# Optimization experiments

Measured on AMD Instinct MI355X. Metric: run time of the kernel, lower is better.

The kernel has to match this reference:

```python
import jax, jax.numpy as jnp
import numpy as np

N_NODES = 100000
N_EDGES = 625000
HIDDEN = 128
N_LAYERS = 4
NUM_GRAPHS = 512
INPUT_DIM = 28
EDGE_DIM = 4
OUT_DIM = 1


def setup_inputs() -> dict:
    key = jax.random.key(0)
    ks = jax.random.split(key, 16)
    x = jax.random.randint(ks[0], (N_NODES, 1), 0, INPUT_DIM)
    edge_index = jax.random.randint(ks[1], (2, N_EDGES), 0, N_NODES)
    edge_attr = jax.random.randint(ks[2], (N_EDGES,), 0, EDGE_DIM)
    batch = jnp.sort(jax.random.randint(ks[3], (N_NODES,), 0, NUM_GRAPHS))
    s = 1.0 / np.sqrt(HIDDEN)
    node_emb = jax.random.normal(ks[4], (INPUT_DIM, HIDDEN), jnp.float32)
    edge_emb = jax.random.normal(ks[5], (EDGE_DIM, HIDDEN), jnp.float32)
    conv_W1 = jax.random.normal(ks[6], (N_LAYERS, HIDDEN, HIDDEN), jnp.float32) * s
    conv_b1 = jnp.zeros((N_LAYERS, HIDDEN), jnp.float32)
    conv_W2 = jax.random.normal(ks[7], (N_LAYERS, HIDDEN, HIDDEN), jnp.float32) * s
    conv_b2 = jnp.zeros((N_LAYERS, HIDDEN), jnp.float32)
    mlp_W1 = jax.random.normal(ks[8], (HIDDEN, HIDDEN // 2), jnp.float32) * s
    mlp_b1 = jnp.zeros((HIDDEN // 2,), jnp.float32)
    mlp_W2 = jax.random.normal(ks[9], (HIDDEN // 2, HIDDEN // 4), jnp.float32) * (1.0 / np.sqrt(HIDDEN // 2))
    mlp_b2 = jnp.zeros((HIDDEN // 4,), jnp.float32)
    mlp_W3 = jax.random.normal(ks[10], (HIDDEN // 4, OUT_DIM), jnp.float32) * (1.0 / np.sqrt(HIDDEN // 4))
    mlp_b3 = jnp.zeros((OUT_DIM,), jnp.float32)
    return dict(x=x, edge_index=edge_index, edge_attr=edge_attr, batch=batch,
                node_emb=node_emb, edge_emb=edge_emb,
                conv_W1=conv_W1, conv_b1=conv_b1, conv_W2=conv_W2, conv_b2=conv_b2,
                mlp_W1=mlp_W1, mlp_b1=mlp_b1, mlp_W2=mlp_W2, mlp_b2=mlp_b2,
                mlp_W3=mlp_W3, mlp_b3=mlp_b3)


def reference(x, edge_index, edge_attr, batch, node_emb, edge_emb,
              conv_W1, conv_b1, conv_W2, conv_b2,
              mlp_W1, mlp_b1, mlp_W2, mlp_b2, mlp_W3, mlp_b3):
    h = node_emb[x[:, 0]]                    # [N, H] embedding lookup (x.squeeze(-1))
    _attr = edge_emb[edge_attr]              # computed in original forward but unused by GINConv
    src, dst = edge_index[0], edge_index[1]
    for l in range(N_LAYERS):
        # GINConv (eps=0): mlp((1+eps)*x + sum_{j->i} x_j)
        agg = jax.ops.segment_sum(h[src], dst, num_segments=N_NODES)  # [N, H]
        z = agg + h
        z = jax.nn.relu(z @ conv_W1[l] + conv_b1[l])
        h = z @ conv_W2[l] + conv_b2[l]
    g = jax.ops.segment_sum(h, batch, num_segments=NUM_GRAPHS)        # global_add_pool [G, H]
    g = jax.nn.relu(g @ mlp_W1 + mlp_b1)
    g = jax.nn.relu(g @ mlp_W2 + mlp_b2)
    return g @ mlp_W3 + mlp_b3               # [G, 1]
```

## Files before the change

### kernel.cpp

```cpp
#include <hip/hip_runtime.h>

#define N_NODES 100000
#define N_EDGES 625000
#define HIDDEN 128
#define NUM_GRAPHS 512
#define CAP 40
#define PADN 100096

typedef unsigned int uint;
typedef unsigned short ushort;
typedef short v8s __attribute__((ext_vector_type(8)));
typedef float v16f __attribute__((ext_vector_type(16)));

__device__ __forceinline__ float b2f_lo(uint u) { return __uint_as_float(u << 16); }
__device__ __forceinline__ float b2f_hi(uint u) { return __uint_as_float(u & 0xffff0000u); }
__device__ __forceinline__ uint f2b(float f) {
  uint u = __float_as_uint(f);
  return (u + 0x7fffu + ((u >> 16) & 1u)) >> 16;
}

__global__ __launch_bounds__(256) void wtrans_k(const float* __restrict__ W1,
                                                const float* __restrict__ W2,
                                                ushort* __restrict__ Wt) {
  int mat = blockIdx.x;
  const float* W = ((mat & 1) ? W2 : W1) + (size_t)(mat >> 1) * 16384;
  ushort* o = Wt + (size_t)mat * 16384;
#pragma unroll
  for (int j = 0; j < 64; j++) {
    int idx = threadIdx.x + 256 * j;
    int k = idx >> 7, n = idx & 127;
    o[n * 128 + k] = (ushort)f2b(W[idx]);
  }
}

__global__ __launch_bounds__(256) void embed_k(const int* __restrict__ x,
                                               const float* __restrict__ emb,
                                               ushort* __restrict__ h) {
  int t = blockIdx.x * 256 + threadIdx.x;
  int n = t >> 4;
  if (n >= N_NODES) return;
  int c = t & 15;
  const float4* e = (const float4*)(emb + (size_t)x[n] * HIDDEN + c * 8);
  float4 a = e[0], b = e[1];
  uint4 o;
  o.x = f2b(a.x) | (f2b(a.y) << 16);
  o.y = f2b(a.z) | (f2b(a.w) << 16);
  o.z = f2b(b.x) | (f2b(b.y) << 16);
  o.w = f2b(b.z) | (f2b(b.w) << 16);
  ((uint4*)h)[t] = o;
}

__global__ __launch_bounds__(256) void build_k(const int* __restrict__ src,
                                               const int* __restrict__ dst,
                                               int* __restrict__ cursor,
                                               int* __restrict__ slots) {
  int e = blockIdx.x * 256 + threadIdx.x;
  if (e >= N_EDGES) return;
  int d = dst[e];
  int p = atomicAdd(&cursor[d], 1);
  if (p < CAP) slots[(size_t)d * CAP + p] = src[e];
}

__global__ __launch_bounds__(256) void hist_k(const int* __restrict__ cursor,
                                              int* __restrict__ bins) {
  __shared__ int lb[CAP + 1];
  int tid = threadIdx.x;
  if (tid <= CAP) lb[tid] = 0;
  __syncthreads();
  int n = blockIdx.x * 256 + tid;
  if (n < N_NODES) {
    int d = cursor[n]; if (d > CAP) d = CAP;
    atomicAdd(&lb[d], 1);
  }
  __syncthreads();
  if (tid <= CAP && lb[tid] > 0) atomicAdd(&bins[tid], lb[tid]);
}

__global__ __launch_bounds__(64) void scan_k(int* __restrict__ bins) {
  int i = threadIdx.x;
  int c = (i <= CAP) ? bins[i] : 0;
  int incl = c;
#pragma unroll
  for (int off = 1; off < 64; off <<= 1) {
    int t = __shfl_up(incl, off, 64);
    if (i >= off) incl += t;
  }
  if (i <= CAP) bins[i] = incl - c;
}

__global__ __launch_bounds__(256) void scatter_k(const int* __restrict__ cursor,
                                                 int* __restrict__ bins,
                                                 int* __restrict__ perm) {
  __shared__ int lb[CAP + 1];
  __shared__ int lbase[CAP + 1];
  int tid = threadIdx.x;
  if (tid <= CAP) lb[tid] = 0;
  __syncthreads();
  int n = blockIdx.x * 256 + tid;
  int d = 0, rank = 0;
  bool real = (n < N_NODES);
  if (real) {
    d = cursor[n]; if (d > CAP) d = CAP;
    rank = atomicAdd(&lb[d], 1);
  }
  __syncthreads();
  if (tid <= CAP) {
    int c = lb[tid];
    lbase[tid] = c > 0 ? atomicAdd(&bins[tid], c) : 0;
  }
  __syncthreads();
  if (real) perm[lbase[d] + rank] = n;
  else if (n < PADN) perm[n] = 0;
}

__device__ __forceinline__ void accum8(const uint4 u[8], float acc[8][8]) {
#pragma unroll
  for (int ks = 0; ks < 8; ks++) {
    acc[ks][0] += b2f_lo(u[ks].x); acc[ks][1] += b2f_hi(u[ks].x);
    acc[ks][2] += b2f_lo(u[ks].y); acc[ks][3] += b2f_hi(u[ks].y);
    acc[ks][4] += b2f_lo(u[ks].z); acc[ks][5] += b2f_hi(u[ks].z);
    acc[ks][6] += b2f_lo(u[ks].w); acc[ks][7] += b2f_hi(u[ks].w);
  }
}

__global__ __launch_bounds__(256, 3) void layer_k(const ushort* __restrict__ hin,
                                                  const int* __restrict__ cursor,
                                                  const int* __restrict__ slots,
                                                  const int* __restrict__ perm,
                                                  const ushort* __restrict__ W1t,
                                                  const ushort* __restrict__ W2t,
                                                  const float* __restrict__ b1,
                                                  const float* __restrict__ b2,
                                                  ushort* __restrict__ hout) {
  __shared__ uint4 Wf[2048];

  int tid = threadIdx.x;
  int lane = tid & 63;
  int wv = tid >> 6;
  int l31 = lane & 31;
  int khalf = lane >> 5;
  int tb = blockIdx.x * 128 + wv * 32;
  int prow = perm[tb + l31];
  bool valid = (tb + l31) < N_NODES;

#pragma unroll
  for (int ks = 0; ks < 8; ks++) {
    const uint4* g = (const uint4*)W1t + ((wv * 32 + l31) << 4) + 2 * ks + khalf;
    __builtin_amdgcn_global_load_lds((const uint*)g, (uint*)(Wf + ((wv * 8 + ks) << 6)), 16, 0, 0);
  }

  float acc[8][8];
#pragma unroll
  for (int ks = 0; ks < 8; ks++)
#pragma unroll
    for (int e = 0; e < 8; e++) acc[ks][e] = 0.f;

  const uint4* base = (const uint4*)hin;
  uint4 cur[8], nxt[8];
  const uint4* rp = base + (size_t)prow * 16;
#pragma unroll
  for (int ks = 0; ks < 8; ks++) cur[ks] = rp[khalf + 2 * ks];

  int deg = valid ? cursor[prow] : 0;
  if (deg > CAP) deg = CAP;
  const int* sl = slots + (size_t)prow * CAP;
  int s = (deg > 0) ? sl[0] : 0;
  for (int j = 0; j < deg; j++) {
    const uint4* np = base + (size_t)s * 16;
#pragma unroll
    for (int ks = 0; ks < 8; ks++) nxt[ks] = np[khalf + 2 * ks];
    s = (j + 1 < deg) ? sl[j + 1] : 0;
    accum8(cur, acc);
#pragma unroll
    for (int ks = 0; ks < 8; ks++) cur[ks] = nxt[ks];
  }
  accum8(cur, acc);

  union U { uint4 u; v8s s; };
  U afr[8];
#pragma unroll
  for (int ks = 0; ks < 8; ks++) {
    afr[ks].u.x = f2b(acc[ks][0]) | (f2b(acc[ks][1]) << 16);
    afr[ks].u.y = f2b(acc[ks][2]) | (f2b(acc[ks][3]) << 16);
    afr[ks].u.z = f2b(acc[ks][4]) | (f2b(acc[ks][5]) << 16);
    afr[ks].u.w = f2b(acc[ks][6]) | (f2b(acc[ks][7]) << 16);
  }

  __syncthreads();

  v16f acc1[4] = {};
#pragma unroll
  for (int c = 0; c < 4; c++)
#pragma unroll
    for (int ks = 0; ks < 8; ks++) {
      U b; b.u = Wf[((c * 8 + ks) << 6) + lane];
      acc1[c] = __builtin_amdgcn_mfma_f32_32x32x16_bf16(b.s, afr[ks].s, acc1[c], 0, 0, 0);
    }

  uint u[4][4][2];
#pragma unroll
  for (int c = 0; c < 4; c++)
#pragma unroll
    for (int b = 0; b < 4; b++)
#pragma unroll
      for (int ap = 0; ap < 2; ap++) {
        int r0 = 2 * ap + 4 * b, r1 = r0 + 1;
        float v0 = fmaxf(acc1[c][r0] + b1[c * 32 + 2 * ap + 8 * b + 4 * khalf], 0.f);
        float v1 = fmaxf(acc1[c][r1] + b1[c * 32 + 2 * ap + 1 + 8 * b + 4 * khalf], 0.f);
        u[c][b][ap] = f2b(v0) | (f2b(v1) << 16);
      }

  uint got[4][2][2];
#pragma unroll
  for (int c = 0; c < 4; c++)
#pragma unroll
    for (int bh = 0; bh < 2; bh++)
#pragma unroll
      for (int ap = 0; ap < 2; ap++) {
        uint send = khalf ? u[c][2 * bh][ap] : u[c][2 * bh + 1][ap];
        got[c][bh][ap] = __shfl_xor(send, 32, 64);
      }

  U az[8];
#pragma unroll
  for (int ks = 0; ks < 8; ks++) {
    uint o0 = khalf ? u[ks >> 1][2 * (ks & 1) + 1][0] : u[ks >> 1][2 * (ks & 1)][0];
    uint o1 = khalf ? u[ks >> 1][2 * (ks & 1) + 1][1] : u[ks >> 1][2 * (ks & 1)][1];
    uint g0 = got[ks >> 1][ks & 1][0];
    uint g1 = got[ks >> 1][ks & 1][1];
    az[ks].u.x = khalf ? g0 : o0;
    az[ks].u.y = khalf ? g1 : o1;
    az[ks].u.z = khalf ? o0 : g0;
    az[ks].u.w = khalf ? o1 : g1;
  }

  __syncthreads();
#pragma unroll
  for (int ks = 0; ks < 8; ks++) {
    const uint4* g = (const uint4*)W2t + ((wv * 32 + l31) << 4) + 2 * ks + khalf;
    __builtin_amdgcn_global_load_lds((const uint*)g, (uint*)(Wf + ((wv * 8 + ks) << 6)), 16, 0, 0);
  }
  __syncthreads();

  v16f acc2[4] = {};
#pragma unroll
  for (int c = 0; c < 4; c++)
#pragma unroll
    for (int ks = 0; ks < 8; ks++) {
      U b; b.u = Wf[((c * 8 + ks) << 6) + lane];
      acc2[c] = __builtin_amdgcn_mfma_f32_32x32x16_bf16(az[ks].s, b.s, acc2[c], 0, 0, 0);
    }

  int trow[16];
#pragma unroll
  for (int r = 0; r < 16; r++) {
    int m = (r & 3) + 8 * (r >> 2) + 4 * khalf;
    trow[r] = __shfl(prow, m, 64);
  }
  float bv2[4];
#pragma unroll
  for (int c = 0; c < 4; c++) bv2[c] = b2[c * 32 + l31];
#pragma unroll
  for (int c = 0; c < 4; c++) {
    int col = c * 32 + l31;
#pragma unroll
    for (int r = 0; r < 16; r++) {
      int m = (r & 3) + 8 * (r >> 2) + 4 * khalf;
      if (tb + m < N_NODES)
        hout[(size_t)trow[r] * HIDDEN + col] = (ushort)f2b(acc2[c][r] + bv2[c]);
    }
  }
}

__global__ __launch_bounds__(256) void poolmlp_k(const ushort* __restrict__ h,
                                                 const int* __restrict__ batch,
                                                 const float* __restrict__ W1, const float* __restrict__ b1,
                                                 const float* __restrict__ W2, const float* __restrict__ b2,
                                                 const float* __restrict__ W3, const float* __restrict__ b3,
                                                 float* __restrict__ out) {
  __shared__ int se[2];
  __shared__ float red[16][16][8];
  __shared__ float gl[128];
  __shared__ float r2[64];
  __shared__ float r3[32];
  int gi = blockIdx.x, tid = threadIdx.x;
  if (tid < 2) {
    int target = gi + tid;
    int lo = 0, hi = N_NODES;
    while (lo < hi) {
      int mid = (lo + hi) >> 1;
      if (batch[mid] < target) lo = mid + 1; else hi = mid;
    }
    se[tid] = lo;
  }
  __syncthreads();
  int start = se[0], end = se[1];
  int cg = tid & 15, rg = tid >> 4;
  float acc[8] = {0.f, 0.f, 0.f, 0.f, 0.f, 0.f, 0.f, 0.f};
  for (int r = start + rg; r < end; r += 16) {
    uint4 v = ((const uint4*)h)[r * 16 + cg];
    acc[0] += b2f_lo(v.x); acc[1] += b2f_hi(v.x);
    acc[2] += b2f_lo(v.y); acc[3] += b2f_hi(v.y);
    acc[4] += b2f_lo(v.z); acc[5] += b2f_hi(v.z);
    acc[6] += b2f_lo(v.w); acc[7] += b2f_hi(v.w);
  }
#pragma unroll
  for (int j = 0; j < 8; j++) red[rg][cg][j] = acc[j];
  __syncthreads();
  if (rg == 0) {
    float s[8];
#pragma unroll
    for (int j = 0; j < 8; j++) s[j] = red[0][cg][j];
#pragma unroll
    for (int i = 1; i < 16; i++)
#pragma unroll
      for (int j = 0; j < 8; j++) s[j] += red[i][cg][j];
#pragma unroll
    for (int j = 0; j < 8; j++) gl[cg * 8 + j] = s[j];
  }
  __syncthreads();
  if (tid < 64) {
    float s = b1[tid];
    for (int k = 0; k < 128; k++) s = fmaf(gl[k], W1[k * 64 + tid], s);
    r2[tid] = fmaxf(s, 0.f);
  }
  __syncthreads();
  if (tid < 32) {
    float s2 = b2[tid];
    for (int k = 0; k < 64; k++) s2 = fmaf(r2[k], W2[k * 32 + tid], s2);
    r3[tid] = fmaxf(s2, 0.f);
  }
  __syncthreads();
  if (tid < 64) {
    float pv = (tid < 32) ? r3[tid] * W3[tid] : 0.f;
#pragma unroll
    for (int off = 32; off > 0; off >>= 1) pv += __shfl_down(pv, off);
    if (tid == 0) out[gi] = pv + b3[0];
  }
}

extern "C" void kernel_launch(void* const* d_in, const int* in_sizes, int n_in,
                              void* d_out, int out_size, void* d_ws, size_t ws_size,
                              hipStream_t stream) {
  const int* x = (const int*)d_in[0];
  const int* src = (const int*)d_in[1];
  const int* dst = src + N_EDGES;
  const int* batch = (const int*)d_in[3];
  const float* node_emb = (const float*)d_in[4];
  const float* cW1 = (const float*)d_in[6];
  const float* cb1 = (const float*)d_in[7];
  const float* cW2 = (const float*)d_in[8];
  const float* cb2 = (const float*)d_in[9];
  const float* mW1 = (const float*)d_in[10];
  const float* mb1 = (const float*)d_in[11];
  const float* mW2 = (const float*)d_in[12];
  const float* mb2 = (const float*)d_in[13];
  const float* mW3 = (const float*)d_in[14];
  const float* mb3 = (const float*)d_in[15];
  float* out = (float*)d_out;

  char* p = (char*)d_ws;
  const size_t HB = (size_t)N_NODES * HIDDEN * sizeof(ushort);
  ushort* h = (ushort*)p;      p += HB;
  ushort* t0 = (ushort*)p;     p += HB;
  ushort* Wtb = (ushort*)p;    p += (size_t)8 * 16384 * sizeof(ushort);
  int* cursor = (int*)p;       p += (size_t)N_NODES * sizeof(int);
  int* bins = (int*)p;         p += 64 * sizeof(int);
  int* slots = (int*)p;        p += (size_t)N_NODES * CAP * sizeof(int);
  int* perm = (int*)p;         p += (size_t)PADN * sizeof(int);

  hipMemsetAsync(cursor, 0, ((size_t)N_NODES + 64) * sizeof(int), stream);
  wtrans_k<<<8, 256, 0, stream>>>(cW1, cW2, Wtb);
  embed_k<<<(N_NODES * 16 + 255) / 256, 256, 0, stream>>>(x, node_emb, h);
  build_k<<<(N_EDGES + 255) / 256, 256, 0, stream>>>(src, dst, cursor, slots);
  hist_k<<<PADN / 256, 256, 0, stream>>>(cursor, bins);
  scan_k<<<1, 64, 0, stream>>>(bins);
  scatter_k<<<PADN / 256, 256, 0, stream>>>(cursor, bins, perm);

  const int grid = PADN / 128;
  ushort* bufs[2] = {h, t0};
  for (int l = 0; l < 4; l++) {
    layer_k<<<grid, 256, 0, stream>>>(bufs[l & 1], cursor, slots, perm,
                                      Wtb + (size_t)(2 * l) * 16384,
                                      Wtb + (size_t)(2 * l + 1) * 16384,
                                      cb1 + (size_t)l * HIDDEN,
                                      cb2 + (size_t)l * HIDDEN,
                                      bufs[(l & 1) ^ 1]);
  }
  poolmlp_k<<<NUM_GRAPHS, 256, 0, stream>>>(h, batch, mW1, mb1, mW2, mb2, mW3, mb3, out);
}
```

Measured before the change: 407.0 us.

## Drop LDS weight staging; read pre-swizzled MFMA weight fragments from global

```diff
diff --git a/kernel.cpp b/kernel.cpp
--- a/kernel.cpp
+++ b/kernel.cpp
@@ -29,7 +29,9 @@
   for (int j = 0; j < 64; j++) {
     int idx = threadIdx.x + 256 * j;
     int k = idx >> 7, n = idx & 127;
-    o[n * 128 + k] = (ushort)f2b(W[idx]);
+    int c = n >> 5, l31 = n & 31;
+    int ks = k >> 4, khalf = (k >> 3) & 1, e = k & 7;
+    o[(((c * 8 + ks) << 6) + (khalf << 5) + l31) * 8 + e] = (ushort)f2b(W[idx]);
   }
 }
 
@@ -123,31 +125,21 @@
   }
 }
 
-__global__ __launch_bounds__(256, 3) void layer_k(const ushort* __restrict__ hin,
-                                                  const int* __restrict__ cursor,
-                                                  const int* __restrict__ slots,
-                                                  const int* __restrict__ perm,
-                                                  const ushort* __restrict__ W1t,
-                                                  const ushort* __restrict__ W2t,
-                                                  const float* __restrict__ b1,
-                                                  const float* __restrict__ b2,
-                                                  ushort* __restrict__ hout) {
-  __shared__ uint4 Wf[2048];
-
-  int tid = threadIdx.x;
-  int lane = tid & 63;
-  int wv = tid >> 6;
+__global__ __launch_bounds__(64, 3) void layer_k(const ushort* __restrict__ hin,
+                                                 const int* __restrict__ cursor,
+                                                 const int* __restrict__ slots,
+                                                 const int* __restrict__ perm,
+                                                 const ushort* __restrict__ W1f,
+                                                 const ushort* __restrict__ W2f,
+                                                 const float* __restrict__ b1,
+                                                 const float* __restrict__ b2,
+                                                 ushort* __restrict__ hout) {
+  int lane = threadIdx.x;
   int l31 = lane & 31;
   int khalf = lane >> 5;
-  int tb = blockIdx.x * 128 + wv * 32;
+  int tb = blockIdx.x * 32;
   int prow = perm[tb + l31];
   bool valid = (tb + l31) < N_NODES;
-
-#pragma unroll
-  for (int ks = 0; ks < 8; ks++) {
-    const uint4* g = (const uint4*)W1t + ((wv * 32 + l31) << 4) + 2 * ks + khalf;
-    __builtin_amdgcn_global_load_lds((const uint*)g, (uint*)(Wf + ((wv * 8 + ks) << 6)), 16, 0, 0);
-  }
 
   float acc[8][8];
 #pragma unroll
@@ -186,14 +178,13 @@
     afr[ks].u.w = f2b(acc[ks][6]) | (f2b(acc[ks][7]) << 16);
   }
 
-  __syncthreads();
-
+  const uint4* W1v = (const uint4*)W1f;
   v16f acc1[4] = {};
 #pragma unroll
   for (int c = 0; c < 4; c++)
 #pragma unroll
     for (int ks = 0; ks < 8; ks++) {
-      U b; b.u = Wf[((c * 8 + ks) << 6) + lane];
+      U b; b.u = W1v[((c * 8 + ks) << 6) + lane];
       acc1[c] = __builtin_amdgcn_mfma_f32_32x32x16_bf16(b.s, afr[ks].s, acc1[c], 0, 0, 0);
     }
 
@@ -234,20 +225,13 @@
     az[ks].u.w = khalf ? o1 : g1;
   }
 
-  __syncthreads();
-#pragma unroll
-  for (int ks = 0; ks < 8; ks++) {
-    const uint4* g = (const uint4*)W2t + ((wv * 32 + l31) << 4) + 2 * ks + khalf;
-    __builtin_amdgcn_global_load_lds((const uint*)g, (uint*)(Wf + ((wv * 8 + ks) << 6)), 16, 0, 0);
-  }
-  __syncthreads();
-
+  const uint4* W2v = (const uint4*)W2f;
   v16f acc2[4] = {};
 #pragma unroll
   for (int c = 0; c < 4; c++)
 #pragma unroll
     for (int ks = 0; ks < 8; ks++) {
-      U b; b.u = Wf[((c * 8 + ks) << 6) + lane];
+      U b; b.u = W2v[((c * 8 + ks) << 6) + lane];
       acc2[c] = __builtin_amdgcn_mfma_f32_32x32x16_bf16(az[ks].s, b.s, acc2[c], 0, 0, 0);
     }
 
@@ -377,15 +361,15 @@
   scan_k<<<1, 64, 0, stream>>>(bins);
   scatter_k<<<PADN / 256, 256, 0, stream>>>(cursor, bins, perm);
 
-  const int grid = PADN / 128;
+  const int grid = PADN / 32;
   ushort* bufs[2] = {h, t0};
   for (int l = 0; l < 4; l++) {
-    layer_k<<<grid, 256, 0, stream>>>(bufs[l & 1], cursor, slots, perm,
-                                      Wtb + (size_t)(2 * l) * 16384,
-                                      Wtb + (size_t)(2 * l + 1) * 16384,
-                                      cb1 + (size_t)l * HIDDEN,
-                                      cb2 + (size_t)l * HIDDEN,
-                                      bufs[(l & 1) ^ 1]);
+    layer_k<<<grid, 64, 0, stream>>>(bufs[l & 1], cursor, slots, perm,
+                                     Wtb + (size_t)(2 * l) * 16384,
+                                     Wtb + (size_t)(2 * l + 1) * 16384,
+                                     cb1 + (size_t)l * HIDDEN,
+                                     cb2 + (size_t)l * HIDDEN,
+                                     bufs[(l & 1) ^ 1]);
   }
   poolmlp_k<<<NUM_GRAPHS, 256, 0, stream>>>(h, batch, mW1, mb1, mW2, mb2, mW3, mb3, out);
 }
```

Result: faster. 363.1 us (-10.8%).
